# Kernel tuning notes

Hardware: AMD Instinct MI355X
Metric: run time of the kernel (lower is better)

## Reference

```python
import jax, jax.numpy as jnp
import numpy as np


def setup_inputs() -> dict:
    key = jax.random.key(0)
    k1, k2 = jax.random.split(key)
    B, H, W, N = 32, 1024, 1024, 96
    output = jax.random.uniform(k1, (B, 1, H, W), dtype=jnp.float32)
    bboxes = jax.random.randint(k2, (B, N, 4), 0, W, dtype=jnp.int32)
    return {"output": output, "bboxes": bboxes}


def reference(output, bboxes):
    # output: [B, 1, H, W] density map; bboxes: [B, N, 4] as (x1, y1, x2, y2).
    B, _, H, W = output.shape
    bb = jnp.clip(bboxes.astype(jnp.int32), 0, W)  # torch: bboxes.long().clip(0, W)
    x = output[:, 0]  # [B, H, W]
    # 2D integral image with zero top/left padding: S[b, i, j] = sum of x[b, :i, :j].
    S = jnp.pad(jnp.cumsum(jnp.cumsum(x, axis=1), axis=2), ((0, 0), (1, 0), (1, 0)))  # [B, H+1, W+1]
    x1, y1, x2, y2 = bb[..., 0], bb[..., 1], bb[..., 2], bb[..., 3]  # each [B, N]
    bidx = jnp.arange(B)[:, None]  # [B, 1] broadcast against [B, N]
    g = lambda yy, xx: S[bidx, yy, xx]
    box_sums = g(y2, x2) - g(y1, x2) - g(y2, x1) + g(y1, x1)  # [B, N]
    # Empty torch slices (x2<=x1 or y2<=y1) sum to 0; mask to match.
    valid = (x2 > x1) & (y2 > y1)
    box_sums = jnp.where(valid, box_sums, jnp.zeros_like(box_sums))
    return jnp.sum(jax.nn.relu(1.0 - box_sums))
```

## Files before the change

kernel.cpp:

```cpp
#include <hip/hip_runtime.h>

#define BATCH 32
#define HDIM 1024
#define WDIM 1024
#define NBOX 96
#define THREADS 256
#define WAVES_PER_BLOCK (THREADS / 64)
#define ROWS_PER_WAVE 4
#define LDS_STRIDE 1088
#define ZERO_SLOT 1087

__device__ __forceinline__ int padidx(int c) { return c + (c >> 4); }

__global__ void zero_ws_kernel(float* __restrict__ ws) {
    int i = blockIdx.x * blockDim.x + threadIdx.x;
    if (i < BATCH * NBOX) ws[i] = 0.0f;
}

__global__ __launch_bounds__(THREADS) void box_accum_kernel(
    const float* __restrict__ img,
    const int* __restrict__ bboxes,
    float* __restrict__ ws_box) {

    __shared__ float lds[WAVES_PER_BLOCK * LDS_STRIDE];

    const int t = threadIdx.x;
    const int lane = t & 63;
    const int wave = t >> 6;
    float* __restrict__ P = lds + wave * LDS_STRIDE;

    const int gwave = blockIdx.x * WAVES_PER_BLOCK + wave;
    const int row0 = gwave * ROWS_PER_WAVE;
    const int b = row0 / HDIM;
    const int hrow0 = row0 - b * HDIM;

    if (lane == 0) P[ZERO_SLOT] = 0.0f;

    const int4* __restrict__ bb = (const int4*)bboxes + b * NBOX;
    int y1a = 0, y2a = 0, ra = 0, la = ZERO_SLOT;
    int y1b = 0, y2b = 0, rb = 0, lb = ZERO_SLOT;
    bool va = false, vb = false;
    {
        int4 q = bb[lane];
        int x1 = min(max(q.x, 0), WDIM), x2 = min(max(q.z, 0), WDIM);
        y1a = min(max(q.y, 0), WDIM);  y2a = min(max(q.w, 0), WDIM);
        va = (x2 > x1);
        if (va) { ra = padidx(x2 - 1); la = (x1 > 0) ? padidx(x1 - 1) : ZERO_SLOT; }
    }
    if (lane < NBOX - 64) {
        int4 q = bb[64 + lane];
        int x1 = min(max(q.x, 0), WDIM), x2 = min(max(q.z, 0), WDIM);
        y1b = min(max(q.y, 0), WDIM);  y2b = min(max(q.w, 0), WDIM);
        vb = (x2 > x1);
        if (vb) { rb = padidx(x2 - 1); lb = (x1 > 0) ? padidx(x1 - 1) : ZERO_SLOT; }
    }

    float acca = 0.0f, accb = 0.0f;
    const float* rowptr = img + (size_t)row0 * WDIM + lane * 16;

    for (int r = 0; r < ROWS_PER_WAVE; ++r) {
        const float4* lp = (const float4*)(rowptr + (size_t)r * WDIM);
        float4 v0 = lp[0], v1 = lp[1], v2 = lp[2], v3 = lp[3];

        float p[16];
        p[0]  = v0.x;        p[1]  = p[0]  + v0.y;
        p[2]  = p[1] + v0.z; p[3]  = p[2]  + v0.w;
        p[4]  = p[3] + v1.x; p[5]  = p[4]  + v1.y;
        p[6]  = p[5] + v1.z; p[7]  = p[6]  + v1.w;
        p[8]  = p[7] + v2.x; p[9]  = p[8]  + v2.y;
        p[10] = p[9] + v2.z; p[11] = p[10] + v2.w;
        p[12] = p[11]+ v3.x; p[13] = p[12] + v3.y;
        p[14] = p[13]+ v3.z; p[15] = p[14] + v3.w;

        float T = p[15];
        float wscan = T;
        #pragma unroll
        for (int off = 1; off < 64; off <<= 1) {
            float u = __shfl_up(wscan, off, 64);
            if (lane >= off) wscan += u;
        }
        float E = wscan - T;

        const int base = 17 * lane;
        #pragma unroll
        for (int j = 0; j < 16; ++j) P[base + j] = E + p[j];

        __builtin_amdgcn_wave_barrier();

        const int row = hrow0 + r;
        if (va && (y1a <= row) && (row < y2a)) acca += P[ra] - P[la];
        if (vb && (y1b <= row) && (row < y2b)) accb += P[rb] - P[lb];

        __builtin_amdgcn_wave_barrier();
    }

    if (va && acca != 0.0f) atomicAdd(&ws_box[b * NBOX + lane], acca);
    if (vb && accb != 0.0f) atomicAdd(&ws_box[b * NBOX + 64 + lane], accb);
}

__global__ void finalize_kernel(const float* __restrict__ ws_box,
                                const int* __restrict__ bboxes,
                                float* __restrict__ out) {
    __shared__ float red[THREADS / 64];
    const int t = threadIdx.x;
    float local = 0.0f;
    for (int idx = t; idx < BATCH * NBOX; idx += THREADS) {
        const int4 q = ((const int4*)bboxes)[idx];
        int x1 = min(max(q.x, 0), WDIM), y1 = min(max(q.y, 0), WDIM);
        int x2 = min(max(q.z, 0), WDIM), y2 = min(max(q.w, 0), WDIM);
        bool valid = (x2 > x1) && (y2 > y1);
        float s = valid ? ws_box[idx] : 0.0f;
        local += fmaxf(1.0f - s, 0.0f);
    }
    #pragma unroll
    for (int off = 32; off > 0; off >>= 1)
        local += __shfl_down(local, off, 64);
    if ((t & 63) == 0) red[t >> 6] = local;
    __syncthreads();
    if (t == 0) {
        float r = 0.0f;
        #pragma unroll
        for (int w = 0; w < THREADS / 64; ++w) r += red[w];
        out[0] = r;
    }
}

extern "C" void kernel_launch(void* const* d_in, const int* in_sizes, int n_in,
                              void* d_out, int out_size, void* d_ws, size_t ws_size,
                              hipStream_t stream) {
    const float* img    = (const float*)d_in[0];
    const int*   bboxes = (const int*)d_in[1];
    float* out = (float*)d_out;
    float* ws_box = (float*)d_ws;

    zero_ws_kernel<<<(BATCH * NBOX + THREADS - 1) / THREADS, THREADS, 0, stream>>>(ws_box);

    const int nblocks = BATCH * HDIM / (ROWS_PER_WAVE * WAVES_PER_BLOCK);
    box_accum_kernel<<<nblocks, THREADS, 0, stream>>>(img, bboxes, ws_box);

    finalize_kernel<<<1, THREADS, 0, stream>>>(ws_box, bboxes, out);
}
```

Baseline: 198.7 us.

## Fuse finalize into accumulation kernel via last-block ticket and prefetch rows

```diff
diff --git a/kernel.cpp b/kernel.cpp
--- a/kernel.cpp
+++ b/kernel.cpp
@@ -5,24 +5,28 @@
 #define WDIM 1024
 #define NBOX 96
 #define THREADS 256
-#define WAVES_PER_BLOCK (THREADS / 64)
+#define WAVES_PER_BLOCK 4
 #define ROWS_PER_WAVE 4
-#define LDS_STRIDE 1088
-#define ZERO_SLOT 1087
+#define NBLOCKS (BATCH * HDIM / (ROWS_PER_WAVE * WAVES_PER_BLOCK))
+#define LDS_STRIDE 1152
+#define ZERO_SLOT 16
 
-__device__ __forceinline__ int padidx(int c) { return c + (c >> 4); }
+__device__ __forceinline__ int padidx(int c) { return c + 2 * (c >> 4); }
 
-__global__ void zero_ws_kernel(float* __restrict__ ws) {
-    int i = blockIdx.x * blockDim.x + threadIdx.x;
-    if (i < BATCH * NBOX) ws[i] = 0.0f;
+__global__ void init_kernel(float* __restrict__ ws) {
+    const int t = threadIdx.x;
+    for (int i = t; i < BATCH * NBOX; i += THREADS) ws[i] = 0.0f;
+    if (t == 0) ((unsigned int*)ws)[BATCH * NBOX] = 0u;
 }
 
 __global__ __launch_bounds__(THREADS) void box_accum_kernel(
     const float* __restrict__ img,
     const int* __restrict__ bboxes,
-    float* __restrict__ ws_box) {
+    float* __restrict__ ws_box,
+    float* __restrict__ out) {
 
     __shared__ float lds[WAVES_PER_BLOCK * LDS_STRIDE];
+    __shared__ unsigned int ticket_s;
 
     const int t = threadIdx.x;
     const int lane = t & 63;
@@ -37,8 +41,8 @@
     if (lane == 0) P[ZERO_SLOT] = 0.0f;
 
     const int4* __restrict__ bb = (const int4*)bboxes + b * NBOX;
-    int y1a = 0, y2a = 0, ra = 0, la = ZERO_SLOT;
-    int y1b = 0, y2b = 0, rb = 0, lb = ZERO_SLOT;
+    int y1a = 0, y2a = 0, ra = ZERO_SLOT, la = ZERO_SLOT;
+    int y1b = 0, y2b = 0, rb = ZERO_SLOT, lb = ZERO_SLOT;
     bool va = false, vb = false;
     {
         int4 q = bb[lane];
@@ -58,19 +62,26 @@
     float acca = 0.0f, accb = 0.0f;
     const float* rowptr = img + (size_t)row0 * WDIM + lane * 16;
 
+    const float4* lp = (const float4*)rowptr;
+    float4 c0 = lp[0], c1 = lp[1], c2 = lp[2], c3 = lp[3];
+
+    #pragma unroll
     for (int r = 0; r < ROWS_PER_WAVE; ++r) {
-        const float4* lp = (const float4*)(rowptr + (size_t)r * WDIM);
-        float4 v0 = lp[0], v1 = lp[1], v2 = lp[2], v3 = lp[3];
+        float4 n0, n1, n2, n3;
+        if (r + 1 < ROWS_PER_WAVE) {
+            const float4* np = (const float4*)(rowptr + (size_t)(r + 1) * WDIM);
+            n0 = np[0]; n1 = np[1]; n2 = np[2]; n3 = np[3];
+        }
 
         float p[16];
-        p[0]  = v0.x;        p[1]  = p[0]  + v0.y;
-        p[2]  = p[1] + v0.z; p[3]  = p[2]  + v0.w;
-        p[4]  = p[3] + v1.x; p[5]  = p[4]  + v1.y;
-        p[6]  = p[5] + v1.z; p[7]  = p[6]  + v1.w;
-        p[8]  = p[7] + v2.x; p[9]  = p[8]  + v2.y;
-        p[10] = p[9] + v2.z; p[11] = p[10] + v2.w;
-        p[12] = p[11]+ v3.x; p[13] = p[12] + v3.y;
-        p[14] = p[13]+ v3.z; p[15] = p[14] + v3.w;
+        p[0]  = c0.x;         p[1]  = p[0]  + c0.y;
+        p[2]  = p[1]  + c0.z; p[3]  = p[2]  + c0.w;
+        p[4]  = p[3]  + c1.x; p[5]  = p[4]  + c1.y;
+        p[6]  = p[5]  + c1.z; p[7]  = p[6]  + c1.w;
+        p[8]  = p[7]  + c2.x; p[9]  = p[8]  + c2.y;
+        p[10] = p[9]  + c2.z; p[11] = p[10] + c2.w;
+        p[12] = p[11] + c3.x; p[13] = p[12] + c3.y;
+        p[14] = p[13] + c3.z; p[15] = p[14] + c3.w;
 
         float T = p[15];
         float wscan = T;
@@ -81,9 +92,10 @@
         }
         float E = wscan - T;
 
-        const int base = 17 * lane;
+        float2* Pw = (float2*)(P + 18 * lane);
         #pragma unroll
-        for (int j = 0; j < 16; ++j) P[base + j] = E + p[j];
+        for (int j = 0; j < 8; ++j)
+            Pw[j] = make_float2(E + p[2 * j], E + p[2 * j + 1]);
 
         __builtin_amdgcn_wave_barrier();
 
@@ -92,36 +104,42 @@
         if (vb && (y1b <= row) && (row < y2b)) accb += P[rb] - P[lb];
 
         __builtin_amdgcn_wave_barrier();
+
+        c0 = n0; c1 = n1; c2 = n2; c3 = n3;
     }
 
     if (va && acca != 0.0f) atomicAdd(&ws_box[b * NBOX + lane], acca);
     if (vb && accb != 0.0f) atomicAdd(&ws_box[b * NBOX + 64 + lane], accb);
-}
 
-__global__ void finalize_kernel(const float* __restrict__ ws_box,
-                                const int* __restrict__ bboxes,
-                                float* __restrict__ out) {
-    __shared__ float red[THREADS / 64];
-    const int t = threadIdx.x;
-    float local = 0.0f;
-    for (int idx = t; idx < BATCH * NBOX; idx += THREADS) {
-        const int4 q = ((const int4*)bboxes)[idx];
-        int x1 = min(max(q.x, 0), WDIM), y1 = min(max(q.y, 0), WDIM);
-        int x2 = min(max(q.z, 0), WDIM), y2 = min(max(q.w, 0), WDIM);
-        bool valid = (x2 > x1) && (y2 > y1);
-        float s = valid ? ws_box[idx] : 0.0f;
-        local += fmaxf(1.0f - s, 0.0f);
-    }
-    #pragma unroll
-    for (int off = 32; off > 0; off >>= 1)
-        local += __shfl_down(local, off, 64);
-    if ((t & 63) == 0) red[t >> 6] = local;
     __syncthreads();
     if (t == 0) {
-        float r = 0.0f;
+        __threadfence();
+        ticket_s = atomicAdd((unsigned int*)(ws_box + BATCH * NBOX), 1u);
+    }
+    __syncthreads();
+    if (ticket_s == NBLOCKS - 1) {
+        __threadfence();
+        float local = 0.0f;
+        const int4* __restrict__ allbb = (const int4*)bboxes;
+        for (int idx = t; idx < BATCH * NBOX; idx += THREADS) {
+            const int4 q = allbb[idx];
+            int x1 = min(max(q.x, 0), WDIM), y1 = min(max(q.y, 0), WDIM);
+            int x2 = min(max(q.z, 0), WDIM), y2 = min(max(q.w, 0), WDIM);
+            bool valid = (x2 > x1) && (y2 > y1);
+            float s = valid ? __hip_atomic_load(&ws_box[idx], __ATOMIC_RELAXED,
+                                                __HIP_MEMORY_SCOPE_AGENT)
+                            : 0.0f;
+            local += fmaxf(1.0f - s, 0.0f);
+        }
         #pragma unroll
-        for (int w = 0; w < THREADS / 64; ++w) r += red[w];
-        out[0] = r;
+        for (int off = 32; off > 0; off >>= 1)
+            local += __shfl_down(local, off, 64);
+        if (lane == 0) lds[wave] = local;
+        __syncthreads();
+        if (t == 0) {
+            float r = lds[0] + lds[1] + lds[2] + lds[3];
+            out[0] = r;
+        }
     }
 }
 
@@ -133,10 +151,6 @@
     float* out = (float*)d_out;
     float* ws_box = (float*)d_ws;
 
-    zero_ws_kernel<<<(BATCH * NBOX + THREADS - 1) / THREADS, THREADS, 0, stream>>>(ws_box);
-
-    const int nblocks = BATCH * HDIM / (ROWS_PER_WAVE * WAVES_PER_BLOCK);
-    box_accum_kernel<<<nblocks, THREADS, 0, stream>>>(img, bboxes, ws_box);
-
-    finalize_kernel<<<1, THREADS, 0, stream>>>(ws_box, bboxes, out);
+    init_kernel<<<1, THREADS, 0, stream>>>(ws_box);
+    box_accum_kernel<<<NBLOCKS, THREADS, 0, stream>>>(img, bboxes, ws_box, out);
 }
```

After: 289.2 us. 45.5% more time.
